# Performance work log

Hardware: AMD Instinct MI355X
Metric: run time of the kernel (lower is better)

## Reference

```python
import jax, jax.numpy as jnp
import numpy as np

# Grid of blocks: blocks[i][j] is Linear(D, D) if mask[i, j] else None.
N_OUT, N_IN, D, B = 8, 8, 128, 32768
BAND = 2  # active blocks: j <= i and i - j <= BAND


def setup_inputs() -> dict:
    key = jax.random.key(0)
    k1, k2, k3 = jax.random.split(key, 3)
    # X: (num input blocks, batch, block feature dim)
    X = jax.random.normal(k1, (N_IN, B, D), dtype=jnp.float32)
    # W[i, j]: torch.nn.Linear weight of block (i, j), shape (out, in)
    W = jax.random.normal(k2, (N_OUT, N_IN, D, D), dtype=jnp.float32) / np.sqrt(D).astype(np.float32)
    b = jax.random.normal(k3, (N_OUT, N_IN, D), dtype=jnp.float32) * 0.01
    i = jnp.arange(N_OUT)[:, None]
    j = jnp.arange(N_IN)[None, :]
    mask = (j <= i) & (i - j <= BAND)  # banded lower-triangular block sparsity
    return {"X": X, "W": W, "b": b, "mask": mask}


def reference(X, W, b, mask):
    # Sequential2D forward: out[i] = sum_j (X[j] @ W[i,j].T + b[i,j]) over active blocks.
    # None blocks contribute a zero vector, which we express by zeroing masked weights/biases.
    m = mask.astype(W.dtype)                       # (i, j)
    Wm = W * m[:, :, None, None]                   # zero out None blocks
    out = jnp.einsum('jbd,ijod->ibo', X, Wm)       # block-row summation of Linear outputs
    bias = jnp.sum(b * m[:, :, None], axis=1)      # (i, o): sum of active biases per row
    return out + bias[:, None, :]                  # (num_out_blocks, batch, block_out)
```

## Files before the change

kernel.cpp:

```cpp
#include <hip/hip_runtime.h>
#include <hip/hip_bf16.h>


#define NOUT  8
#define NIN   8
#define DD    128
#define BATCH 32768
#define BAND  2

#define BM 128
#define BN 128
#define BK 64
#define SK (BK + 8)

typedef __attribute__((ext_vector_type(8))) short  short8;
typedef __attribute__((ext_vector_type(4))) float  floatx4;

__device__ __forceinline__ unsigned short f2bf(float f) {
    unsigned int u = __float_as_uint(f);
    u += 0x7fffu + ((u >> 16) & 1u);
    return (unsigned short)(u >> 16);
}

__device__ __forceinline__ short8 pack8(floatx4 f0, floatx4 f1) {
    short8 p;
    p[0] = (short)f2bf(f0[0]); p[1] = (short)f2bf(f0[1]);
    p[2] = (short)f2bf(f0[2]); p[3] = (short)f2bf(f0[3]);
    p[4] = (short)f2bf(f1[0]); p[5] = (short)f2bf(f1[1]);
    p[6] = (short)f2bf(f1[2]); p[7] = (short)f2bf(f1[3]);
    return p;
}

__global__ __launch_bounds__(512)
void seq2d_kernel(const float* __restrict__ X,
                  const float* __restrict__ W,
                  const float* __restrict__ Bv,
                  float* __restrict__ out) {
    const int i  = blockIdx.y;
    const int m0 = blockIdx.x * BM;

    __shared__ unsigned short sA[BM * SK];
    __shared__ unsigned short sB[BN * SK];
    __shared__ float sbias[DD];

    const int tid  = threadIdx.x;
    const int lane = tid & 63;
    const int wave = tid >> 6;
    const int wm   = (wave & 1) * 64;
    const int wn   = (wave >> 1) * 32;
    const int l15  = lane & 15;
    const int quad = lane >> 4;

    int jlo = i - BAND; if (jlo < 0) jlo = 0;
    const int nc = (i - jlo + 1) * 2;

    if (tid < DD) {
        float s = 0.f;
        for (int j = jlo; j <= i; ++j)
            s += Bv[(i * NIN + j) * DD + tid];
        sbias[tid] = s;
    }

    floatx4 acc[4][2];
#pragma unroll
    for (int a = 0; a < 4; ++a)
#pragma unroll
        for (int c = 0; c < 2; ++c)
            acc[a][c] = (floatx4){0.f, 0.f, 0.f, 0.f};

    const int srow = tid >> 3;
    const int scol = (tid & 7) << 3;

    floatx4 pa[4], pb[4];

    auto prefetch = [&](int c) {
        const int j  = jlo + (c >> 1);
        const int k0 = (c & 1) * BK;
        const float* __restrict__ xa =
            X + (size_t)j * BATCH * DD + (size_t)(m0 + srow) * DD + k0 + scol;
        pa[0] = *(const floatx4*)(xa);
        pa[1] = *(const floatx4*)(xa + 4);
        pa[2] = *(const floatx4*)(xa + 64 * DD);
        pa[3] = *(const floatx4*)(xa + 64 * DD + 4);
        const float* __restrict__ wb =
            W + (size_t)(i * NIN + j) * DD * DD + (size_t)srow * DD + k0 + scol;
        pb[0] = *(const floatx4*)(wb);
        pb[1] = *(const floatx4*)(wb + 4);
        pb[2] = *(const floatx4*)(wb + 64 * DD);
        pb[3] = *(const floatx4*)(wb + 64 * DD + 4);
    };

    prefetch(0);

    for (int c = 0; c < nc; ++c) {
        __syncthreads();
        *(short8*)(&sA[srow * SK + scol])        = pack8(pa[0], pa[1]);
        *(short8*)(&sA[(64 + srow) * SK + scol]) = pack8(pa[2], pa[3]);
        *(short8*)(&sB[srow * SK + scol])        = pack8(pb[0], pb[1]);
        *(short8*)(&sB[(64 + srow) * SK + scol]) = pack8(pb[2], pb[3]);
        if (c + 1 < nc) prefetch(c + 1);
        __syncthreads();

#pragma unroll
        for (int kk = 0; kk < BK; kk += 32) {
            short8 af[4], bfr[2];
#pragma unroll
            for (int t = 0; t < 4; ++t)
                af[t] = *(const short8*)(&sA[(wm + t * 16 + l15) * SK + kk + quad * 8]);
#pragma unroll
            for (int t = 0; t < 2; ++t)
                bfr[t] = *(const short8*)(&sB[(wn + t * 16 + l15) * SK + kk + quad * 8]);
#pragma unroll
            for (int mt = 0; mt < 4; ++mt)
#pragma unroll
                for (int nt = 0; nt < 2; ++nt)
                    acc[mt][nt] = __builtin_amdgcn_mfma_f32_16x16x32_bf16(
                        af[mt], bfr[nt], acc[mt][nt], 0, 0, 0);
        }
    }

    float* outi = out + (size_t)i * BATCH * DD;
#pragma unroll
    for (int mt = 0; mt < 4; ++mt) {
#pragma unroll
        for (int nt = 0; nt < 2; ++nt) {
            const int n_g  = wn + nt * 16 + l15;
            const float bs = sbias[n_g];
            const int m_b  = m0 + wm + mt * 16 + quad * 4;
#pragma unroll
            for (int r = 0; r < 4; ++r)
                outi[(size_t)(m_b + r) * DD + n_g] = acc[mt][nt][r] + bs;
        }
    }
}

extern "C" void kernel_launch(void* const* d_in, const int* in_sizes, int n_in,
                              void* d_out, int out_size, void* d_ws, size_t ws_size,
                              hipStream_t stream) {
    const float* X  = (const float*)d_in[0];
    const float* W  = (const float*)d_in[1];
    const float* Bv = (const float*)d_in[2];
    float* out = (float*)d_out;

    dim3 grid(BATCH / BM, NOUT);
    seq2d_kernel<<<grid, 512, 0, stream>>>(X, W, Bv, out);
}
```

Before: 261.3 us.

## Load X straight into registers as MFMA fragments and stage only W in LDS

Activations X are no longer staged through shared memory. Each wave loads its own 32-row slice of X directly into registers in MFMA fragment layout, double-buffered and prefetched one k-step ahead. Only the full 128x128 weight block per j is converted to bf16 and stored in LDS. Block size drops to 256 threads with 3 blocks per SM requested, and each wave computes a 32x128 output tile. This removes the LDS round trip and half the barriers for X, at the cost of more accumulator registers and W loads that are not overlapped with compute.

```diff
diff --git a/kernel.cpp b/kernel.cpp
--- a/kernel.cpp
+++ b/kernel.cpp
@@ -1,5 +1,4 @@
 #include <hip/hip_runtime.h>
-#include <hip/hip_bf16.h>
 
 
 #define NOUT  8
@@ -8,10 +7,9 @@
 #define BATCH 32768
 #define BAND  2
 
-#define BM 128
-#define BN 128
-#define BK 64
-#define SK (BK + 8)
+#define BM    128
+#define WROWS 32
+#define SKW   136
 
 typedef __attribute__((ext_vector_type(8))) short  short8;
 typedef __attribute__((ext_vector_type(4))) float  floatx4;
@@ -31,7 +29,7 @@
     return p;
 }
 
-__global__ __launch_bounds__(512)
+__global__ __launch_bounds__(256, 3)
 void seq2d_kernel(const float* __restrict__ X,
                   const float* __restrict__ W,
                   const float* __restrict__ Bv,
@@ -39,20 +37,34 @@
     const int i  = blockIdx.y;
     const int m0 = blockIdx.x * BM;
 
-    __shared__ unsigned short sA[BM * SK];
-    __shared__ unsigned short sB[BN * SK];
+    __shared__ unsigned short sW[DD * SKW];
     __shared__ float sbias[DD];
 
     const int tid  = threadIdx.x;
     const int lane = tid & 63;
     const int wave = tid >> 6;
-    const int wm   = (wave & 1) * 64;
-    const int wn   = (wave >> 1) * 32;
     const int l15  = lane & 15;
     const int quad = lane >> 4;
+    const int wrow = wave * WROWS;
 
     int jlo = i - BAND; if (jlo < 0) jlo = 0;
-    const int nc = (i - jlo + 1) * 2;
+    const int ncs = (i - jlo + 1) * 4;
+
+    const float* xb = X + (size_t)(m0 + wrow + l15) * DD + quad * 8;
+
+    floatx4 px[2][2][2];
+
+    auto prefetch = [&](int par, int c) {
+        const int j  = jlo + (c >> 2);
+        const int k0 = (c & 3) * 32;
+        const float* p = xb + (size_t)j * (BATCH * DD) + k0;
+        px[par][0][0] = *(const floatx4*)(p);
+        px[par][0][1] = *(const floatx4*)(p + 4);
+        px[par][1][0] = *(const floatx4*)(p + 16 * DD);
+        px[par][1][1] = *(const floatx4*)(p + 16 * DD + 4);
+    };
+
+    prefetch(0, 0);
 
     if (tid < DD) {
         float s = 0.f;
@@ -61,75 +73,66 @@
         sbias[tid] = s;
     }
 
-    floatx4 acc[4][2];
+    floatx4 acc[2][8];
 #pragma unroll
-    for (int a = 0; a < 4; ++a)
+    for (int a = 0; a < 2; ++a)
 #pragma unroll
-        for (int c = 0; c < 2; ++c)
-            acc[a][c] = (floatx4){0.f, 0.f, 0.f, 0.f};
+        for (int n = 0; n < 8; ++n)
+            acc[a][n] = (floatx4){0.f, 0.f, 0.f, 0.f};
 
-    const int srow = tid >> 3;
-    const int scol = (tid & 7) << 3;
+    const int wr_r = tid >> 3;
+    const int wr_c = (tid & 7) << 4;
 
-    floatx4 pa[4], pb[4];
-
-    auto prefetch = [&](int c) {
-        const int j  = jlo + (c >> 1);
-        const int k0 = (c & 1) * BK;
-        const float* __restrict__ xa =
-            X + (size_t)j * BATCH * DD + (size_t)(m0 + srow) * DD + k0 + scol;
-        pa[0] = *(const floatx4*)(xa);
-        pa[1] = *(const floatx4*)(xa + 4);
-        pa[2] = *(const floatx4*)(xa + 64 * DD);
-        pa[3] = *(const floatx4*)(xa + 64 * DD + 4);
-        const float* __restrict__ wb =
-            W + (size_t)(i * NIN + j) * DD * DD + (size_t)srow * DD + k0 + scol;
-        pb[0] = *(const floatx4*)(wb);
-        pb[1] = *(const floatx4*)(wb + 4);
-        pb[2] = *(const floatx4*)(wb + 64 * DD);
-        pb[3] = *(const floatx4*)(wb + 64 * DD + 4);
-    };
-
-    prefetch(0);
-
-    for (int c = 0; c < nc; ++c) {
+    int c = 0;
+    for (int j = jlo; j <= i; ++j) {
+        const float* wsrc = W + (size_t)(i * NIN + j) * DD * DD;
         __syncthreads();
-        *(short8*)(&sA[srow * SK + scol])        = pack8(pa[0], pa[1]);
-        *(short8*)(&sA[(64 + srow) * SK + scol]) = pack8(pa[2], pa[3]);
-        *(short8*)(&sB[srow * SK + scol])        = pack8(pb[0], pb[1]);
-        *(short8*)(&sB[(64 + srow) * SK + scol]) = pack8(pb[2], pb[3]);
-        if (c + 1 < nc) prefetch(c + 1);
+#pragma unroll
+        for (int p = 0; p < 4; ++p) {
+            const int r = p * 32 + wr_r;
+            const float* wp = wsrc + (size_t)r * DD + wr_c;
+            floatx4 w0 = *(const floatx4*)(wp);
+            floatx4 w1 = *(const floatx4*)(wp + 4);
+            floatx4 w2 = *(const floatx4*)(wp + 8);
+            floatx4 w3 = *(const floatx4*)(wp + 12);
+            *(short8*)&sW[r * SKW + wr_c]     = pack8(w0, w1);
+            *(short8*)&sW[r * SKW + wr_c + 8] = pack8(w2, w3);
+        }
         __syncthreads();
 
 #pragma unroll
-        for (int kk = 0; kk < BK; kk += 32) {
-            short8 af[4], bfr[2];
+        for (int ks = 0; ks < 4; ++ks) {
+            const int par = ks & 1;
+            if (c + 1 < ncs) prefetch(par ^ 1, c + 1);
+
+            short8 a0 = pack8(px[par][0][0], px[par][0][1]);
+            short8 a1 = pack8(px[par][1][0], px[par][1][1]);
+
+            short8 bf[8];
 #pragma unroll
-            for (int t = 0; t < 4; ++t)
-                af[t] = *(const short8*)(&sA[(wm + t * 16 + l15) * SK + kk + quad * 8]);
+            for (int nf = 0; nf < 8; ++nf)
+                bf[nf] = *(const short8*)&sW[(nf * 16 + l15) * SKW + ks * 32 + quad * 8];
+
 #pragma unroll
-            for (int t = 0; t < 2; ++t)
-                bfr[t] = *(const short8*)(&sB[(wn + t * 16 + l15) * SK + kk + quad * 8]);
-#pragma unroll
-            for (int mt = 0; mt < 4; ++mt)
-#pragma unroll
-                for (int nt = 0; nt < 2; ++nt)
-                    acc[mt][nt] = __builtin_amdgcn_mfma_f32_16x16x32_bf16(
-                        af[mt], bfr[nt], acc[mt][nt], 0, 0, 0);
+            for (int nf = 0; nf < 8; ++nf) {
+                acc[0][nf] = __builtin_amdgcn_mfma_f32_16x16x32_bf16(a0, bf[nf], acc[0][nf], 0, 0, 0);
+                acc[1][nf] = __builtin_amdgcn_mfma_f32_16x16x32_bf16(a1, bf[nf], acc[1][nf], 0, 0, 0);
+            }
+            ++c;
         }
     }
 
     float* outi = out + (size_t)i * BATCH * DD;
 #pragma unroll
-    for (int mt = 0; mt < 4; ++mt) {
+    for (int mf = 0; mf < 2; ++mf) {
 #pragma unroll
-        for (int nt = 0; nt < 2; ++nt) {
-            const int n_g  = wn + nt * 16 + l15;
+        for (int nf = 0; nf < 8; ++nf) {
+            const int n_g  = nf * 16 + l15;
             const float bs = sbias[n_g];
-            const int m_b  = m0 + wm + mt * 16 + quad * 4;
+            const int m_b  = m0 + wrow + mf * 16 + quad * 4;
 #pragma unroll
             for (int r = 0; r < 4; ++r)
-                outi[(size_t)(m_b + r) * DD + n_g] = acc[mt][nt][r] + bs;
+                outi[(size_t)(m_b + r) * DD + n_g] = acc[mf][nf][r] + bs;
         }
     }
 }
@@ -143,5 +146,5 @@
     float* out = (float*)d_out;
 
     dim3 grid(BATCH / BM, NOUT);
-    seq2d_kernel<<<grid, 512, 0, stream>>>(X, W, Bv, out);
+    seq2d_kernel<<<grid, 256, 0, stream>>>(X, W, Bv, out);
 }
```

After: 271.4 us. 1.04x slower.
